# Performance work log

Measured on AMD Instinct MI355X. Metric: run time of the kernel, lower is better.

Reference implementation:

```python
import jax, jax.numpy as jnp
import numpy as np

N_NEURON = 500_000
N_EDGE = 10_000_000
TAO_D = 2.0
TAO_R = 10.0
DT = 0.1
LAMDA_D = DT / TAO_D  # dt/tao_d
LAMDA_R = DT / TAO_R  # dt/tao_r


def setup_inputs() -> dict:
    key = jax.random.key(0)
    ks = jax.random.split(key, 8)
    edges = jax.random.randint(ks[0], (2, N_EDGE), 0, N_NEURON, dtype=jnp.int64)  # row0=post, row1=pre
    return {
        "weight": jax.random.normal(ks[1], (N_EDGE,), dtype=jnp.float32),
        "edges": edges,
        "Iback": jax.random.normal(ks[2], (N_NEURON,), dtype=jnp.float32),
        "spike": jax.random.uniform(ks[3], (N_NEURON,), dtype=jnp.float32),
        "s": jax.random.normal(ks[4], (N_NEURON,), dtype=jnp.float32),
        "r": jax.random.normal(ks[5], (N_NEURON,), dtype=jnp.float32),
        "noise": jax.random.normal(ks[6], (N_NEURON,), dtype=jnp.float32),
        "dt_over_tau": jax.random.uniform(ks[7], (1,), dtype=jnp.float32),
        "sqrt_coeff": jnp.ones((1,), dtype=jnp.float32),
        "sig": jnp.ones((1,), dtype=jnp.float32),
        "mu": jnp.zeros((1,), dtype=jnp.float32),
    }


def reference(weight, edges, Iback, spike, s, r, noise, dt_over_tau, sqrt_coeff, sig, mu):
    # OU background-current update + effective input current
    Iback_new = Iback + dt_over_tau * (noise - Iback)
    Ieff = Iback_new / sqrt_coeff * sig + mu
    # dual-exponential synaptic trace updates
    s_new = s + LAMDA_R * (-s + spike / TAO_D)
    r_new = r - LAMDA_D * r + DT * s_new
    # sparse COO matvec: I[post] += w_e * r_new[pre]
    post, pre = edges[0], edges[1]
    I = jax.ops.segment_sum(weight * r_new[pre], post, num_segments=N_NEURON) + Ieff
    return I
```

## Files before the change

### kernel.cpp

```cpp
#include <hip/hip_runtime.h>
#include <hip/hip_fp16.h>

#define N_NEURON 500000
#define N_EDGE   10000000

#define DT_C      0.1f
#define LAMDA_D_C 0.05f
#define LAMDA_R_C 0.01f
#define INV_TAO_D 0.5f

#define BUCKET_SHIFT 11
#define BUCKET_W     (1 << BUCKET_SHIFT)
#define NBUCKET      ((N_NEURON + BUCKET_W - 1) >> BUCKET_SHIFT)

#define P1_BLOCK 512
#define P1_EPT   16
#define P1_CHUNK (P1_BLOCK * P1_EPT)
#define NCHUNK   ((N_EDGE + P1_CHUNK - 1) / P1_CHUNK)
#define OFFS_STRIDE 256

#define WS_RNEW_OFF  0u
#define WS_OFFS_OFF  (2u * 1024u * 1024u)
#define WS_REC_OFF   (4u * 1024u * 1024u)
#define WS_NEEDED    ((size_t)WS_REC_OFF + (size_t)NCHUNK * P1_CHUNK * 4u)

__device__ __forceinline__ unsigned pack_rec(int post, float v) {
    const unsigned short hv = __half_as_ushort(__float2half_rn(v));
    return ((unsigned)hv << 16) | ((unsigned)post & (BUCKET_W - 1));
}
__device__ __forceinline__ float rec_val(unsigned rec) {
    return __half2float(__ushort_as_half((unsigned short)(rec >> 16)));
}

__global__ void neuron_update(const float4* __restrict__ Iback,
                              const float4* __restrict__ spike,
                              const float4* __restrict__ s,
                              const float4* __restrict__ r,
                              const float4* __restrict__ noise,
                              const float* __restrict__ dt_over_tau,
                              const float* __restrict__ sqrt_coeff,
                              const float* __restrict__ sig,
                              const float* __restrict__ mu,
                              float4* __restrict__ r_new,
                              float4* __restrict__ out,
                              int n4) {
    const float dtau = dt_over_tau[0];
    const float sq   = sqrt_coeff[0];
    const float sg   = sig[0];
    const float m    = mu[0];
    const int i = blockIdx.x * blockDim.x + threadIdx.x;
    if (i >= n4) return;
    const float4 ib = Iback[i], no = noise[i], sv = s[i], sp = spike[i], rv = r[i];
    float4 ieff, rn;
    {
        float a;
        a = ib.x + dtau * (no.x - ib.x); ieff.x = a / sq * sg + m;
        a = ib.y + dtau * (no.y - ib.y); ieff.y = a / sq * sg + m;
        a = ib.z + dtau * (no.z - ib.z); ieff.z = a / sq * sg + m;
        a = ib.w + dtau * (no.w - ib.w); ieff.w = a / sq * sg + m;
        float sn;
        sn = sv.x + LAMDA_R_C * (-sv.x + sp.x * INV_TAO_D); rn.x = rv.x - LAMDA_D_C * rv.x + DT_C * sn;
        sn = sv.y + LAMDA_R_C * (-sv.y + sp.y * INV_TAO_D); rn.y = rv.y - LAMDA_D_C * rv.y + DT_C * sn;
        sn = sv.z + LAMDA_R_C * (-sv.z + sp.z * INV_TAO_D); rn.z = rv.z - LAMDA_D_C * rv.z + DT_C * sn;
        sn = sv.w + LAMDA_R_C * (-sv.w + sp.w * INV_TAO_D); rn.w = rv.w - LAMDA_D_C * rv.w + DT_C * sn;
    }
    r_new[i] = rn;
    out[i]   = ieff;
}

__global__ __launch_bounds__(P1_BLOCK, 8) void edge_bin(
        const float* __restrict__ weight,
        const int*   __restrict__ post_arr,
        const int*   __restrict__ pre_arr,
        const float* __restrict__ r_new,
        unsigned*    __restrict__ records,
        unsigned*    __restrict__ offs,
        int n_edge) {
    __shared__ unsigned rec_lds[P1_CHUNK];
    __shared__ unsigned cnt[NBUCKET];
    __shared__ unsigned lbase[NBUCKET + 1];

    const int t      = threadIdx.x;
    const int chunk0 = blockIdx.x * P1_CHUNK;

    for (int i = t; i < NBUCKET; i += P1_BLOCK) cnt[i] = 0;
    __syncthreads();

    #pragma unroll
    for (int k = 0; k < P1_EPT / 4; ++k) {
        const int e = chunk0 + (k * P1_BLOCK + t) * 4;
        if (e < n_edge) {
            const int4 p4 = *reinterpret_cast<const int4*>(post_arr + e);
            atomicAdd(&cnt[((unsigned)p4.x) >> BUCKET_SHIFT], 1u);
            atomicAdd(&cnt[((unsigned)p4.y) >> BUCKET_SHIFT], 1u);
            atomicAdd(&cnt[((unsigned)p4.z) >> BUCKET_SHIFT], 1u);
            atomicAdd(&cnt[((unsigned)p4.w) >> BUCKET_SHIFT], 1u);
        }
    }
    __syncthreads();

    if (t < 64) {
        unsigned carry = 0;
        #pragma unroll
        for (int c = 0; c < 4; ++c) {
            const int idx = c * 64 + t;
            unsigned v = (idx < NBUCKET) ? cnt[idx] : 0u;
            const unsigned orig = v;
            #pragma unroll
            for (int d = 1; d < 64; d <<= 1) {
                const unsigned u = __shfl_up(v, d);
                if (t >= d) v += u;
            }
            if (idx <= NBUCKET) lbase[idx] = carry + v - orig;
            carry += __shfl(v, 63);
        }
    }
    __syncthreads();

    for (int i = t; i < NBUCKET; i += P1_BLOCK) cnt[i] = 0;
    __syncthreads();

    #pragma unroll
    for (int k = 0; k < P1_EPT / 4; ++k) {
        const int e = chunk0 + (k * P1_BLOCK + t) * 4;
        if (e < n_edge) {
            const int4   p4 = *reinterpret_cast<const int4*>(post_arr + e);
            const int4   q4 = *reinterpret_cast<const int4*>(pre_arr + e);
            const float4 w4 = *reinterpret_cast<const float4*>(weight + e);
            const int   ps[4] = {p4.x, p4.y, p4.z, p4.w};
            const int   qs[4] = {q4.x, q4.y, q4.z, q4.w};
            const float wv[4] = {w4.x, w4.y, w4.z, w4.w};
            #pragma unroll
            for (int j = 0; j < 4; ++j) {
                const unsigned b = ((unsigned)ps[j]) >> BUCKET_SHIFT;
                const unsigned l = atomicAdd(&cnt[b], 1u);
                rec_lds[lbase[b] + l] = pack_rec(ps[j], wv[j] * r_new[qs[j]]);
            }
        }
    }
    __syncthreads();

    if (t <= NBUCKET)
        offs[blockIdx.x * OFFS_STRIDE + t] = lbase[t];
    const unsigned total = lbase[NBUCKET];
    unsigned* dst = records + (size_t)blockIdx.x * P1_CHUNK;
    for (unsigned i = t; i < total; i += P1_BLOCK)
        dst[i] = rec_lds[i];
}

__global__ __launch_bounds__(1024) void bucket_reduce(
        const unsigned* __restrict__ records,
        const unsigned* __restrict__ offs,
        float*          __restrict__ out,
        int n, int nchunk) {
    __shared__ float acc[BUCKET_W];
    const int b = blockIdx.x;
    const int t = threadIdx.x;
    for (int i = t; i < BUCKET_W; i += 1024) acc[i] = 0.f;
    __syncthreads();

    const int grp = t >> 5, lane = t & 31;
    for (int j = grp; j < nchunk; j += 32) {
        const unsigned s0 = offs[j * OFFS_STRIDE + b];
        const unsigned e0 = offs[j * OFFS_STRIDE + b + 1];
        const unsigned* src = records + (size_t)j * P1_CHUNK;
        for (unsigned i = s0 + lane; i < e0; i += 32) {
            const unsigned rec = src[i];
            atomicAdd(&acc[rec & (BUCKET_W - 1)], rec_val(rec));
        }
    }
    __syncthreads();

    const int g0 = b << BUCKET_SHIFT;
    for (int i = t; i < BUCKET_W; i += 1024) {
        const int g = g0 + i;
        if (g < n) out[g] += acc[i];
    }
}

__global__ void edge_scatter(const float* __restrict__ weight,
                             const int* __restrict__ post,
                             const int* __restrict__ pre,
                             const float* __restrict__ r_new,
                             float* __restrict__ out,
                             int n_edge) {
    for (int e = blockIdx.x * blockDim.x + threadIdx.x; e < n_edge;
         e += gridDim.x * blockDim.x) {
        atomicAdd(&out[post[e]], weight[e] * r_new[pre[e]]);
    }
}

extern "C" void kernel_launch(void* const* d_in, const int* in_sizes, int n_in,
                              void* d_out, int out_size, void* d_ws, size_t ws_size,
                              hipStream_t stream) {
    const float* weight      = (const float*)d_in[0];
    const int*   edges       = (const int*)d_in[1];
    const float* Iback       = (const float*)d_in[2];
    const float* spike       = (const float*)d_in[3];
    const float* s           = (const float*)d_in[4];
    const float* r           = (const float*)d_in[5];
    const float* noise       = (const float*)d_in[6];
    const float* dt_over_tau = (const float*)d_in[7];
    const float* sqrt_coeff  = (const float*)d_in[8];
    const float* sig         = (const float*)d_in[9];
    const float* mu          = (const float*)d_in[10];

    float* out = (float*)d_out;
    char*  ws  = (char*)d_ws;

    float*    r_new   = (float*)(ws + WS_RNEW_OFF);
    unsigned* offs    = (unsigned*)(ws + WS_OFFS_OFF);
    unsigned* records = (unsigned*)(ws + WS_REC_OFF);

    const int n_edge = in_sizes[0];
    const int n      = out_size;

    {
        const int n4    = n / 4;
        const int block = 256;
        const int grid  = (n4 + block - 1) / block;
        neuron_update<<<grid, block, 0, stream>>>(
            (const float4*)Iback, (const float4*)spike, (const float4*)s,
            (const float4*)r, (const float4*)noise,
            dt_over_tau, sqrt_coeff, sig, mu,
            (float4*)r_new, (float4*)out, n4);
    }

    const int nchunk = (n_edge + P1_CHUNK - 1) / P1_CHUNK;

    if (ws_size >= WS_NEEDED) {
        edge_bin<<<nchunk, P1_BLOCK, 0, stream>>>(
            weight, edges, edges + n_edge, r_new, records, offs, n_edge);

        bucket_reduce<<<NBUCKET, 1024, 0, stream>>>(records, offs, out, n, nchunk);
    } else {
        edge_scatter<<<4096, 256, 0, stream>>>(
            weight, edges, edges + n_edge, r_new, out, n_edge);
    }
}
```

Baseline: 123.9 us.

## Single-pass edge binning with register-held records; fuse Ieff into bucket reduce

The edge binning kernel now reads post, pre and weight once. Each edge's packed record and its bucket/slot metadata stay in registers between the count pass and the scatter pass, so the second global read of the edge arrays and the count reset are gone. The Ieff computation moves from the neuron update kernel into the final bucket reduction, which avoids writing out and then reading it back. This raises register use per thread in the binning kernel (32 extra values), which may reduce occupancy.

```diff
diff --git a/kernel.cpp b/kernel.cpp
--- a/kernel.cpp
+++ b/kernel.cpp
@@ -18,6 +18,7 @@
 #define P1_CHUNK (P1_BLOCK * P1_EPT)
 #define NCHUNK   ((N_EDGE + P1_CHUNK - 1) / P1_CHUNK)
 #define OFFS_STRIDE 256
+#define META_NONE 0xFFFFFFFFu
 
 #define WS_RNEW_OFF  0u
 #define WS_OFFS_OFF  (2u * 1024u * 1024u)
@@ -32,40 +33,21 @@
     return __half2float(__ushort_as_half((unsigned short)(rec >> 16)));
 }
 
-__global__ void neuron_update(const float4* __restrict__ Iback,
-                              const float4* __restrict__ spike,
-                              const float4* __restrict__ s,
-                              const float4* __restrict__ r,
-                              const float4* __restrict__ noise,
-                              const float* __restrict__ dt_over_tau,
-                              const float* __restrict__ sqrt_coeff,
-                              const float* __restrict__ sig,
-                              const float* __restrict__ mu,
-                              float4* __restrict__ r_new,
-                              float4* __restrict__ out,
-                              int n4) {
-    const float dtau = dt_over_tau[0];
-    const float sq   = sqrt_coeff[0];
-    const float sg   = sig[0];
-    const float m    = mu[0];
+__global__ void neuron_update_r(const float4* __restrict__ spike,
+                                const float4* __restrict__ s,
+                                const float4* __restrict__ r,
+                                float4* __restrict__ r_new,
+                                int n4) {
     const int i = blockIdx.x * blockDim.x + threadIdx.x;
     if (i >= n4) return;
-    const float4 ib = Iback[i], no = noise[i], sv = s[i], sp = spike[i], rv = r[i];
-    float4 ieff, rn;
-    {
-        float a;
-        a = ib.x + dtau * (no.x - ib.x); ieff.x = a / sq * sg + m;
-        a = ib.y + dtau * (no.y - ib.y); ieff.y = a / sq * sg + m;
-        a = ib.z + dtau * (no.z - ib.z); ieff.z = a / sq * sg + m;
-        a = ib.w + dtau * (no.w - ib.w); ieff.w = a / sq * sg + m;
-        float sn;
-        sn = sv.x + LAMDA_R_C * (-sv.x + sp.x * INV_TAO_D); rn.x = rv.x - LAMDA_D_C * rv.x + DT_C * sn;
-        sn = sv.y + LAMDA_R_C * (-sv.y + sp.y * INV_TAO_D); rn.y = rv.y - LAMDA_D_C * rv.y + DT_C * sn;
-        sn = sv.z + LAMDA_R_C * (-sv.z + sp.z * INV_TAO_D); rn.z = rv.z - LAMDA_D_C * rv.z + DT_C * sn;
-        sn = sv.w + LAMDA_R_C * (-sv.w + sp.w * INV_TAO_D); rn.w = rv.w - LAMDA_D_C * rv.w + DT_C * sn;
-    }
+    const float4 sv = s[i], sp = spike[i], rv = r[i];
+    float4 rn;
+    float sn;
+    sn = sv.x + LAMDA_R_C * (-sv.x + sp.x * INV_TAO_D); rn.x = rv.x - LAMDA_D_C * rv.x + DT_C * sn;
+    sn = sv.y + LAMDA_R_C * (-sv.y + sp.y * INV_TAO_D); rn.y = rv.y - LAMDA_D_C * rv.y + DT_C * sn;
+    sn = sv.z + LAMDA_R_C * (-sv.z + sp.z * INV_TAO_D); rn.z = rv.z - LAMDA_D_C * rv.z + DT_C * sn;
+    sn = sv.w + LAMDA_R_C * (-sv.w + sp.w * INV_TAO_D); rn.w = rv.w - LAMDA_D_C * rv.w + DT_C * sn;
     r_new[i] = rn;
-    out[i]   = ieff;
 }
 
 __global__ __launch_bounds__(P1_BLOCK, 8) void edge_bin(
@@ -86,15 +68,29 @@
     for (int i = t; i < NBUCKET; i += P1_BLOCK) cnt[i] = 0;
     __syncthreads();
 
+    unsigned rec[P1_EPT];
+    unsigned meta[P1_EPT];
+
     #pragma unroll
     for (int k = 0; k < P1_EPT / 4; ++k) {
         const int e = chunk0 + (k * P1_BLOCK + t) * 4;
         if (e < n_edge) {
-            const int4 p4 = *reinterpret_cast<const int4*>(post_arr + e);
-            atomicAdd(&cnt[((unsigned)p4.x) >> BUCKET_SHIFT], 1u);
-            atomicAdd(&cnt[((unsigned)p4.y) >> BUCKET_SHIFT], 1u);
-            atomicAdd(&cnt[((unsigned)p4.z) >> BUCKET_SHIFT], 1u);
-            atomicAdd(&cnt[((unsigned)p4.w) >> BUCKET_SHIFT], 1u);
+            const int4   p4 = *reinterpret_cast<const int4*>(post_arr + e);
+            const int4   q4 = *reinterpret_cast<const int4*>(pre_arr + e);
+            const float4 w4 = *reinterpret_cast<const float4*>(weight + e);
+            const int   ps[4] = {p4.x, p4.y, p4.z, p4.w};
+            const int   qs[4] = {q4.x, q4.y, q4.z, q4.w};
+            const float wv[4] = {w4.x, w4.y, w4.z, w4.w};
+            #pragma unroll
+            for (int j = 0; j < 4; ++j) {
+                const unsigned b = ((unsigned)ps[j]) >> BUCKET_SHIFT;
+                const unsigned l = atomicAdd(&cnt[b], 1u);
+                rec[k * 4 + j]  = pack_rec(ps[j], wv[j] * r_new[qs[j]]);
+                meta[k * 4 + j] = (b << 13) | l;
+            }
+        } else {
+            #pragma unroll
+            for (int j = 0; j < 4; ++j) meta[k * 4 + j] = META_NONE;
         }
     }
     __syncthreads();
@@ -117,26 +113,10 @@
     }
     __syncthreads();
 
-    for (int i = t; i < NBUCKET; i += P1_BLOCK) cnt[i] = 0;
-    __syncthreads();
-
     #pragma unroll
-    for (int k = 0; k < P1_EPT / 4; ++k) {
-        const int e = chunk0 + (k * P1_BLOCK + t) * 4;
-        if (e < n_edge) {
-            const int4   p4 = *reinterpret_cast<const int4*>(post_arr + e);
-            const int4   q4 = *reinterpret_cast<const int4*>(pre_arr + e);
-            const float4 w4 = *reinterpret_cast<const float4*>(weight + e);
-            const int   ps[4] = {p4.x, p4.y, p4.z, p4.w};
-            const int   qs[4] = {q4.x, q4.y, q4.z, q4.w};
-            const float wv[4] = {w4.x, w4.y, w4.z, w4.w};
-            #pragma unroll
-            for (int j = 0; j < 4; ++j) {
-                const unsigned b = ((unsigned)ps[j]) >> BUCKET_SHIFT;
-                const unsigned l = atomicAdd(&cnt[b], 1u);
-                rec_lds[lbase[b] + l] = pack_rec(ps[j], wv[j] * r_new[qs[j]]);
-            }
-        }
+    for (int k = 0; k < P1_EPT; ++k) {
+        if (meta[k] != META_NONE)
+            rec_lds[lbase[meta[k] >> 13] + (meta[k] & 0x1FFFu)] = rec[k];
     }
     __syncthreads();
 
@@ -151,6 +131,12 @@
 __global__ __launch_bounds__(1024) void bucket_reduce(
         const unsigned* __restrict__ records,
         const unsigned* __restrict__ offs,
+        const float* __restrict__ Iback,
+        const float* __restrict__ noise,
+        const float* __restrict__ dt_over_tau,
+        const float* __restrict__ sqrt_coeff,
+        const float* __restrict__ sig,
+        const float* __restrict__ mu,
         float*          __restrict__ out,
         int n, int nchunk) {
     __shared__ float acc[BUCKET_W];
@@ -171,10 +157,43 @@
     }
     __syncthreads();
 
+    const float dtau = dt_over_tau[0];
+    const float sq   = sqrt_coeff[0];
+    const float sg   = sig[0];
+    const float m    = mu[0];
     const int g0 = b << BUCKET_SHIFT;
     for (int i = t; i < BUCKET_W; i += 1024) {
         const int g = g0 + i;
-        if (g < n) out[g] += acc[i];
+        if (g < n) {
+            const float ib   = Iback[g];
+            const float ibn  = ib + dtau * (noise[g] - ib);
+            out[g] = acc[i] + (ibn / sq * sg + m);
+        }
+    }
+}
+
+__global__ void neuron_update_full(const float* __restrict__ Iback,
+                                   const float* __restrict__ spike,
+                                   const float* __restrict__ s,
+                                   const float* __restrict__ r,
+                                   const float* __restrict__ noise,
+                                   const float* __restrict__ dt_over_tau,
+                                   const float* __restrict__ sqrt_coeff,
+                                   const float* __restrict__ sig,
+                                   const float* __restrict__ mu,
+                                   float* __restrict__ r_new,
+                                   float* __restrict__ out,
+                                   int n) {
+    const float dtau = dt_over_tau[0], sq = sqrt_coeff[0], sg = sig[0], m = mu[0];
+    for (int i = blockIdx.x * blockDim.x + threadIdx.x; i < n;
+         i += gridDim.x * blockDim.x) {
+        float ib  = Iback[i];
+        float ibn = ib + dtau * (noise[i] - ib);
+        float sv  = s[i];
+        float sn  = sv + LAMDA_R_C * (-sv + spike[i] * INV_TAO_D);
+        float rv  = r[i];
+        r_new[i] = rv - LAMDA_D_C * rv + DT_C * sn;
+        out[i]   = ibn / sq * sg + m;
     }
 }
 
@@ -215,25 +234,25 @@
     const int n_edge = in_sizes[0];
     const int n      = out_size;
 
-    {
-        const int n4    = n / 4;
-        const int block = 256;
-        const int grid  = (n4 + block - 1) / block;
-        neuron_update<<<grid, block, 0, stream>>>(
-            (const float4*)Iback, (const float4*)spike, (const float4*)s,
-            (const float4*)r, (const float4*)noise,
-            dt_over_tau, sqrt_coeff, sig, mu,
-            (float4*)r_new, (float4*)out, n4);
-    }
-
     const int nchunk = (n_edge + P1_CHUNK - 1) / P1_CHUNK;
 
     if (ws_size >= WS_NEEDED) {
+        {
+            const int n4 = n / 4;
+            neuron_update_r<<<(n4 + 255) / 256, 256, 0, stream>>>(
+                (const float4*)spike, (const float4*)s, (const float4*)r,
+                (float4*)r_new, n4);
+        }
         edge_bin<<<nchunk, P1_BLOCK, 0, stream>>>(
             weight, edges, edges + n_edge, r_new, records, offs, n_edge);
 
-        bucket_reduce<<<NBUCKET, 1024, 0, stream>>>(records, offs, out, n, nchunk);
+        bucket_reduce<<<NBUCKET, 1024, 0, stream>>>(
+            records, offs, Iback, noise, dt_over_tau, sqrt_coeff, sig, mu,
+            out, n, nchunk);
     } else {
+        neuron_update_full<<<(n + 255) / 256, 256, 0, stream>>>(
+            Iback, spike, s, r, noise, dt_over_tau, sqrt_coeff, sig, mu,
+            r_new, out, n);
         edge_scatter<<<4096, 256, 0, stream>>>(
             weight, edges, edges + n_edge, r_new, out, n_edge);
     }
```

Result: no change. 121.7 us (-1.7%).
